# Kernel optimization log

Measured on AMD Instinct MI355X. Metric: run time of the kernel, lower is better.

The kernel has to match this reference:

```python
import jax, jax.numpy as jnp
import numpy as np

B = 2097152  # flattened batch of 3x3 rotation matrices

def setup_inputs() -> dict:
    key = jax.random.key(0)
    k1, k2 = jax.random.split(key)
    # scale by 0.1 so cos=(trace(m1 m2^T)-1)/2 stays strictly inside (-1,1)
    pred_rot = jax.random.normal(k1, (B, 3, 3), dtype=jnp.float32) * 0.1
    gt_rot = jax.random.normal(k2, (B, 3, 3), dtype=jnp.float32) * 0.1
    return {"pred_rot": pred_rot, "gt_rot": gt_rot}

def reference(pred_rot, gt_rot):
    m1 = pred_rot.reshape(-1, 3, 3)
    m2 = gt_rot.reshape(-1, 3, 3)
    # trace(m1 @ m2^T) == sum(m1 * m2) elementwise -> avoid the bmm
    cos = (jnp.einsum('bij,bij->b', m1, m2) - 1.0) * 0.5
    cos = jnp.clip(cos, -1.0, 1.0)  # min with +1, max with -1
    theta = jnp.arccos(cos)
    return jnp.mean(theta)  # reduction='mean'
```

## Files before the change

kernel.cpp:

```cpp
#include <hip/hip_runtime.h>
#include <math.h>


#define TPB 256
#define NBLOCKS 2048

__global__ __launch_bounds__(TPB) void geo_kernel(
    const float* __restrict__ a, const float* __restrict__ b,
    float* __restrict__ out, float invM, int M)
{
    __shared__ float wsum[TPB / 64];
    const int tid = threadIdx.x;
    float sum = 0.0f;

    const long long G    = (long long)M >> 2;
    const long long gid0 = (long long)blockIdx.x * TPB + tid;
    const long long gstr = (long long)gridDim.x * TPB;

    for (long long g = gid0; g < G; g += gstr) {
        const float4* __restrict__ pa = (const float4*)a + 9 * g;
        const float4* __restrict__ pb = (const float4*)b + 9 * g;
        const float4 A0 = pa[0], A1 = pa[1], A2 = pa[2], A3 = pa[3], A4 = pa[4],
                     A5 = pa[5], A6 = pa[6], A7 = pa[7], A8 = pa[8];
        const float4 B0 = pb[0], B1 = pb[1], B2 = pb[2], B3 = pb[3], B4 = pb[4],
                     B5 = pb[5], B6 = pb[6], B7 = pb[7], B8 = pb[8];

        float d0 = A0.x * B0.x;
        d0 = fmaf(A0.y, B0.y, d0); d0 = fmaf(A0.z, B0.z, d0);
        d0 = fmaf(A0.w, B0.w, d0);
        d0 = fmaf(A1.x, B1.x, d0); d0 = fmaf(A1.y, B1.y, d0);
        d0 = fmaf(A1.z, B1.z, d0); d0 = fmaf(A1.w, B1.w, d0);
        d0 = fmaf(A2.x, B2.x, d0);

        float d1 = A2.y * B2.y;
        d1 = fmaf(A2.z, B2.z, d1); d1 = fmaf(A2.w, B2.w, d1);
        d1 = fmaf(A3.x, B3.x, d1); d1 = fmaf(A3.y, B3.y, d1);
        d1 = fmaf(A3.z, B3.z, d1); d1 = fmaf(A3.w, B3.w, d1);
        d1 = fmaf(A4.x, B4.x, d1); d1 = fmaf(A4.y, B4.y, d1);

        float d2 = A4.z * B4.z;
        d2 = fmaf(A4.w, B4.w, d2);
        d2 = fmaf(A5.x, B5.x, d2); d2 = fmaf(A5.y, B5.y, d2);
        d2 = fmaf(A5.z, B5.z, d2); d2 = fmaf(A5.w, B5.w, d2);
        d2 = fmaf(A6.x, B6.x, d2); d2 = fmaf(A6.y, B6.y, d2);
        d2 = fmaf(A6.z, B6.z, d2);

        float d3 = A6.w * B6.w;
        d3 = fmaf(A7.x, B7.x, d3); d3 = fmaf(A7.y, B7.y, d3);
        d3 = fmaf(A7.z, B7.z, d3); d3 = fmaf(A7.w, B7.w, d3);
        d3 = fmaf(A8.x, B8.x, d3); d3 = fmaf(A8.y, B8.y, d3);
        d3 = fmaf(A8.z, B8.z, d3); d3 = fmaf(A8.w, B8.w, d3);

        sum += acosf(fminf(1.0f, fmaxf(-1.0f, (d0 - 1.0f) * 0.5f)));
        sum += acosf(fminf(1.0f, fmaxf(-1.0f, (d1 - 1.0f) * 0.5f)));
        sum += acosf(fminf(1.0f, fmaxf(-1.0f, (d2 - 1.0f) * 0.5f)));
        sum += acosf(fminf(1.0f, fmaxf(-1.0f, (d3 - 1.0f) * 0.5f)));
    }

    for (long long m = 4 * G + gid0; m < M; m += gstr) {
        float d = 0.0f;
        #pragma unroll
        for (int j = 0; j < 9; ++j)
            d = fmaf(a[m * 9 + j], b[m * 9 + j], d);
        sum += acosf(fminf(1.0f, fmaxf(-1.0f, (d - 1.0f) * 0.5f)));
    }

    #pragma unroll
    for (int off = 32; off > 0; off >>= 1)
        sum += __shfl_down(sum, off, 64);
    const int lane = tid & 63;
    const int wid  = tid >> 6;
    if (lane == 0) wsum[wid] = sum;
    __syncthreads();
    if (tid == 0) {
        float s = 0.0f;
        #pragma unroll
        for (int i = 0; i < TPB / 64; ++i) s += wsum[i];
        atomicAdd(out, s * invM);
    }
}

extern "C" void kernel_launch(void* const* d_in, const int* in_sizes, int n_in,
                              void* d_out, int out_size, void* d_ws, size_t ws_size,
                              hipStream_t stream) {
    const float* a = (const float*)d_in[0];
    const float* b = (const float*)d_in[1];
    float* out = (float*)d_out;

    const int n = in_sizes[0];
    const int M = n / 9;

    hipMemsetAsync(out, 0, (size_t)out_size * sizeof(float), stream);
    geo_kernel<<<NBLOCKS, TPB, 0, stream>>>(a, b, out, 1.0f / (float)M, M);
}
```

Before: 169.7 us.

## Coalesce loads across lanes and regroup matrix products through per-wave LDS

Each thread used to read 9 contiguous float4s, so lanes accessed strided addresses. Now each lane reads float4s with a 64-element stride, so every wave load instruction is fully coalesced. The elementwise products go to a per-wave LDS scratch buffer, and each lane then reads back 9 floats per matrix to sum four matrices. This adds LDS traffic, LDS bank conflicts on the stride-9 reads, and 36KB of shared memory per block, which may reduce occupancy.

Result: no change. 169.0 us (-0.5%).

```diff
diff --git a/kernel.cpp b/kernel.cpp
--- a/kernel.cpp
+++ b/kernel.cpp
@@ -4,73 +4,78 @@
 
 #define TPB 256
 #define NBLOCKS 2048
+#define MPW 256
+#define MPB 1024
+#define W4_PER_WAVE 576
+#define LDSF_PER_WAVE 2304
 
 __global__ __launch_bounds__(TPB) void geo_kernel(
     const float* __restrict__ a, const float* __restrict__ b,
     float* __restrict__ out, float invM, int M)
 {
+    __shared__ float prod[4 * LDSF_PER_WAVE];
     __shared__ float wsum[TPB / 64];
-    const int tid = threadIdx.x;
+
+    const int tid  = threadIdx.x;
+    const int lane = tid & 63;
+    const int wv   = tid >> 6;
+    float* lp = prod + wv * LDSF_PER_WAVE;
+
     float sum = 0.0f;
+    const long long NT = (long long)M / MPB;
 
-    const long long G    = (long long)M >> 2;
-    const long long gid0 = (long long)blockIdx.x * TPB + tid;
-    const long long gstr = (long long)gridDim.x * TPB;
+    for (long long t = blockIdx.x; t < NT; t += gridDim.x) {
+        const long long base4 = t * (9LL * MPB / 4) + wv * W4_PER_WAVE + lane;
+        const float4* __restrict__ pa = (const float4*)a + base4;
+        const float4* __restrict__ pb = (const float4*)b + base4;
+        const float4 A0 = pa[0],   A1 = pa[64],  A2 = pa[128],
+                     A3 = pa[192], A4 = pa[256], A5 = pa[320],
+                     A6 = pa[384], A7 = pa[448], A8 = pa[512];
+        const float4 B0 = pb[0],   B1 = pb[64],  B2 = pb[128],
+                     B3 = pb[192], B4 = pb[256], B5 = pb[320],
+                     B6 = pb[384], B7 = pb[448], B8 = pb[512];
 
-    for (long long g = gid0; g < G; g += gstr) {
-        const float4* __restrict__ pa = (const float4*)a + 9 * g;
-        const float4* __restrict__ pb = (const float4*)b + 9 * g;
-        const float4 A0 = pa[0], A1 = pa[1], A2 = pa[2], A3 = pa[3], A4 = pa[4],
-                     A5 = pa[5], A6 = pa[6], A7 = pa[7], A8 = pa[8];
-        const float4 B0 = pb[0], B1 = pb[1], B2 = pb[2], B3 = pb[3], B4 = pb[4],
-                     B5 = pb[5], B6 = pb[6], B7 = pb[7], B8 = pb[8];
+        #define PK(k)                                                       \
+        {                                                                   \
+            float4 p;                                                       \
+            p.x = A##k.x * B##k.x; p.y = A##k.y * B##k.y;                   \
+            p.z = A##k.z * B##k.z; p.w = A##k.w * B##k.w;                   \
+            *(float4*)&lp[4 * (64 * (k) + lane)] = p;                       \
+        }
+        PK(0) PK(1) PK(2) PK(3) PK(4) PK(5) PK(6) PK(7) PK(8)
+        #undef PK
 
-        float d0 = A0.x * B0.x;
-        d0 = fmaf(A0.y, B0.y, d0); d0 = fmaf(A0.z, B0.z, d0);
-        d0 = fmaf(A0.w, B0.w, d0);
-        d0 = fmaf(A1.x, B1.x, d0); d0 = fmaf(A1.y, B1.y, d0);
-        d0 = fmaf(A1.z, B1.z, d0); d0 = fmaf(A1.w, B1.w, d0);
-        d0 = fmaf(A2.x, B2.x, d0);
+        asm volatile("s_waitcnt lgkmcnt(0)" ::: "memory");
 
-        float d1 = A2.y * B2.y;
-        d1 = fmaf(A2.z, B2.z, d1); d1 = fmaf(A2.w, B2.w, d1);
-        d1 = fmaf(A3.x, B3.x, d1); d1 = fmaf(A3.y, B3.y, d1);
-        d1 = fmaf(A3.z, B3.z, d1); d1 = fmaf(A3.w, B3.w, d1);
-        d1 = fmaf(A4.x, B4.x, d1); d1 = fmaf(A4.y, B4.y, d1);
+        #pragma unroll
+        for (int q = 0; q < 4; ++q) {
+            const float* r = lp + 9 * (64 * q + lane);
+            float d = ((r[0] + r[1]) + (r[2] + r[3])) +
+                      ((r[4] + r[5]) + (r[6] + r[7])) + r[8];
+            float cv = fminf(1.0f, fmaxf(-1.0f, (d - 1.0f) * 0.5f));
+            sum += acosf(cv);
+        }
 
-        float d2 = A4.z * B4.z;
-        d2 = fmaf(A4.w, B4.w, d2);
-        d2 = fmaf(A5.x, B5.x, d2); d2 = fmaf(A5.y, B5.y, d2);
-        d2 = fmaf(A5.z, B5.z, d2); d2 = fmaf(A5.w, B5.w, d2);
-        d2 = fmaf(A6.x, B6.x, d2); d2 = fmaf(A6.y, B6.y, d2);
-        d2 = fmaf(A6.z, B6.z, d2);
-
-        float d3 = A6.w * B6.w;
-        d3 = fmaf(A7.x, B7.x, d3); d3 = fmaf(A7.y, B7.y, d3);
-        d3 = fmaf(A7.z, B7.z, d3); d3 = fmaf(A7.w, B7.w, d3);
-        d3 = fmaf(A8.x, B8.x, d3); d3 = fmaf(A8.y, B8.y, d3);
-        d3 = fmaf(A8.z, B8.z, d3); d3 = fmaf(A8.w, B8.w, d3);
-
-        sum += acosf(fminf(1.0f, fmaxf(-1.0f, (d0 - 1.0f) * 0.5f)));
-        sum += acosf(fminf(1.0f, fmaxf(-1.0f, (d1 - 1.0f) * 0.5f)));
-        sum += acosf(fminf(1.0f, fmaxf(-1.0f, (d2 - 1.0f) * 0.5f)));
-        sum += acosf(fminf(1.0f, fmaxf(-1.0f, (d3 - 1.0f) * 0.5f)));
+        asm volatile("s_waitcnt lgkmcnt(0)" ::: "memory");
     }
 
-    for (long long m = 4 * G + gid0; m < M; m += gstr) {
-        float d = 0.0f;
-        #pragma unroll
-        for (int j = 0; j < 9; ++j)
-            d = fmaf(a[m * 9 + j], b[m * 9 + j], d);
-        sum += acosf(fminf(1.0f, fmaxf(-1.0f, (d - 1.0f) * 0.5f)));
+    {
+        const long long gid    = (long long)blockIdx.x * TPB + tid;
+        const long long stride = (long long)gridDim.x * TPB;
+        for (long long m = NT * MPB + gid; m < M; m += stride) {
+            float d = 0.0f;
+            #pragma unroll
+            for (int j = 0; j < 9; ++j)
+                d = fmaf(a[m * 9 + j], b[m * 9 + j], d);
+            float cv = fminf(1.0f, fmaxf(-1.0f, (d - 1.0f) * 0.5f));
+            sum += acosf(cv);
+        }
     }
 
     #pragma unroll
     for (int off = 32; off > 0; off >>= 1)
         sum += __shfl_down(sum, off, 64);
-    const int lane = tid & 63;
-    const int wid  = tid >> 6;
-    if (lane == 0) wsum[wid] = sum;
+    if ((tid & 63) == 0) wsum[tid >> 6] = sum;
     __syncthreads();
     if (tid == 0) {
         float s = 0.0f;
```
